# Kernel optimization log

Measured on AMD Instinct MI355X. Metric: run time of the kernel, lower is better.

## Reference

```python
import jax, jax.numpy as jnp
import numpy as np

HID = 64
CTX = 64
STEPS = 2
RANK = 16
NODES = 1024
B, T = 16, 24
EPS = 1e-5


def _linear(x, W, b):
    # torch nn.Linear: x @ W.T + b, W is [out, in]
    return jnp.einsum('...i,oi->...o', x, W) + b


def _gelu(x):
    return jax.nn.gelu(x, approximate=False)


def _diffusion(adj, state, Ws, bs):
    # Ws: [S, out, in], bs: [S, out]
    term = jnp.zeros_like(state)
    for s in range(Ws.shape[0]):
        state = jnp.einsum('nm,btmf->btnf', adj, state)
        term = term + _linear(state, Ws[s], bs[s])
    return term


def setup_inputs() -> dict:
    key = jax.random.key(0)
    ks = jax.random.split(key, 32)
    f32 = jnp.float32
    def w(k, *shape, scale=None):
        s = scale if scale is not None else 1.0 / np.sqrt(shape[-1])
        return jax.random.uniform(k, shape, f32, -s, s)
    inp = {
        'x': jax.random.normal(ks[0], (B, T, NODES, HID), f32),
        'a_fwd': jax.random.uniform(ks[1], (NODES, NODES), f32),
        'context': jax.random.normal(ks[2], (B, T, NODES, CTX), f32),
        'W_self': w(ks[3], HID, HID), 'b_self': w(ks[4], HID),
        'W_fwd': w(ks[5], STEPS, HID, HID), 'b_fwd': w(ks[6], STEPS, HID),
        'W_bwd': w(ks[7], STEPS, HID, HID), 'b_bwd': w(ks[8], STEPS, HID),
        'W_adp': w(ks[9], STEPS, HID, HID), 'b_adp': w(ks[10], STEPS, HID),
        'Wg1': w(ks[11], HID, CTX), 'bg1': w(ks[12], HID),
        'Wg2': w(ks[13], 4, HID), 'bg2': w(ks[14], 4),
        'Ws1': w(ks[15], HID, CTX), 'bs1': w(ks[16], HID),
        'Ws2': w(ks[17], HID, HID), 'bs2': w(ks[18], HID),
        'W_src': w(ks[19], 1, CTX), 'b_src': w(ks[20], 1),
        'W_dst': w(ks[21], 1, CTX), 'b_dst': w(ks[22], 1),
        'emb_src': jax.random.normal(ks[23], (NODES, RANK), f32) * 0.02,
        'emb_dst': jax.random.normal(ks[24], (NODES, RANK), f32) * 0.02,
        'gamma': jnp.ones((HID,), f32), 'beta': jnp.zeros((HID,), f32),
    }
    return inp


def reference(x, a_fwd, context, W_self, b_self, W_fwd, b_fwd, W_bwd, b_bwd,
              W_adp, b_adp, Wg1, bg1, Wg2, bg2, Ws1, bs1, Ws2, bs2,
              W_src, b_src, W_dst, b_dst, emb_src, emb_dst, gamma, beta):
    a_bwd = a_fwd.T
    # adaptive adjacency: softmax(relu(Es @ Ed^T)) over last dim
    a_adp = jax.nn.softmax(jax.nn.relu(emb_src @ emb_dst.T), axis=-1)

    gates = jax.nn.sigmoid(_linear(_gelu(_linear(context, Wg1, bg1)), Wg2, bg2))  # [b,t,n,4]
    scale = jax.nn.sigmoid(_linear(_gelu(_linear(context, Ws1, bs1)), Ws2, bs2))  # [b,t,n,F]
    src_gate = jax.nn.sigmoid(_linear(context, W_src, b_src))  # [b,t,n,1]
    dst_gate = jax.nn.sigmoid(_linear(context, W_dst, b_dst))  # [b,t,n,1]

    self_term = _linear(x, W_self, b_self)
    fwd_term = _diffusion(a_fwd, x * dst_gate, W_fwd, b_fwd)
    bwd_term = _diffusion(a_bwd, x * src_gate, W_bwd, b_bwd)
    adp_term = _diffusion(a_adp, x, W_adp, b_adp)

    mixed = (gates[..., 0:1] * self_term + gates[..., 1:2] * fwd_term
             + gates[..., 2:3] * bwd_term + gates[..., 3:4] * adp_term) * scale

    h = x + _gelu(mixed)  # dropout is identity in eval mode
    mu = jnp.mean(h, axis=-1, keepdims=True)
    var = jnp.mean(jnp.square(h - mu), axis=-1, keepdims=True)
    return (h - mu) * jax.lax.rsqrt(var + EPS) * gamma + beta
```

## Files before the change

### kernel.cpp

```cpp
#include <hip/hip_runtime.h>
#include <math.h>

typedef unsigned short u16;
typedef short short8 __attribute__((ext_vector_type(8)));
typedef float f32x4 __attribute__((ext_vector_type(4)));

#define LN_EPS 1e-5f

__device__ __forceinline__ float gelu_exact(float x){
    return 0.5f * x * (1.0f + erff(x * 0.70710678118654752f));
}
__device__ __forceinline__ float sigmoidf_(float x){
    return 1.0f / (1.0f + __expf(-x));
}
__device__ __forceinline__ u16 f2bf(float f){
    unsigned u = __float_as_uint(f);
    u += 0x7fffu + ((u >> 16) & 1u);
    return (u16)(u >> 16);
}
__device__ __forceinline__ float b2f(u16 u){
    return __uint_as_float(((unsigned)u) << 16);
}

#define GLLDS(gp, lp) __builtin_amdgcn_global_load_lds( \
    (const __attribute__((address_space(1))) unsigned int*)(const void*)(gp), \
    (__attribute__((address_space(3))) unsigned int*)(void*)(lp), 16, 0, 0)

__global__ __launch_bounds__(256) void k_prep(
    const float* __restrict__ Wg1, const float* __restrict__ Ws1,
    const float* __restrict__ Ws2, const float* __restrict__ Wself,
    const float* __restrict__ Wg2, const float* __restrict__ Wsrc,
    const float* __restrict__ Wdst, const float* __restrict__ Wfwd,
    const float* __restrict__ Wbwd, const float* __restrict__ Wadp,
    u16* __restrict__ wbf)
{
    const int i = blockIdx.x*256 + threadIdx.x;
    if (i >= 41344) return;
    const float* src; int off;
    if      (i < 4096)  { src = Wg1;  off = 0; }
    else if (i < 8192)  { src = Ws1;  off = 4096; }
    else if (i < 12288) { src = Ws2;  off = 8192; }
    else if (i < 16384) { src = Wself;off = 12288; }
    else if (i < 24576) { src = Wfwd; off = 16384; }
    else if (i < 32768) { src = Wbwd; off = 24576; }
    else if (i < 40960) { src = Wadp; off = 32768; }
    else if (i < 41216) { src = Wg2;  off = 40960; }
    else if (i < 41280) { src = Wsrc; off = 41216; }
    else                { src = Wdst; off = 41280; }
    wbf[i] = f2bf(src[i - off]);
}

__global__ __launch_bounds__(256) void k_adp(const float* __restrict__ es,
                                             const float* __restrict__ ed,
                                             u16* __restrict__ aadp){
    __shared__ float srow[1024];
    __shared__ float s_es[16];
    __shared__ float sredm[4];
    __shared__ float sreds[4];
    const int n   = blockIdx.x;
    const int tid = threadIdx.x;
    const int wid = tid >> 6, lane = tid & 63;
    if (tid < 16) s_es[tid] = es[n*16 + tid];
    __syncthreads();
    float lmax = 0.0f;
    for (int m = tid; m < 1024; m += 256){
        const float* edm = ed + m*16;
        float z = 0.f;
        #pragma unroll
        for (int r = 0; r < 16; r++) z = fmaf(s_es[r], edm[r], z);
        z = fmaxf(z, 0.0f);
        srow[m] = z;
        lmax = fmaxf(lmax, z);
    }
    #pragma unroll
    for (int o = 32; o > 0; o >>= 1) lmax = fmaxf(lmax, __shfl_xor(lmax, o, 64));
    if (lane == 0) sredm[wid] = lmax;
    __syncthreads();
    const float tmax = fmaxf(fmaxf(sredm[0], sredm[1]), fmaxf(sredm[2], sredm[3]));
    float lsum = 0.f;
    for (int m = tid; m < 1024; m += 256){
        float e = expf(srow[m] - tmax);
        srow[m] = e;
        lsum += e;
    }
    #pragma unroll
    for (int o = 32; o > 0; o >>= 1) lsum += __shfl_xor(lsum, o, 64);
    if (lane == 0) sreds[wid] = lsum;
    __syncthreads();
    const float inv = 1.0f / (sreds[0] + sreds[1] + sreds[2] + sreds[3]);
    for (int m = tid; m < 1024; m += 256) aadp[(size_t)n*1024 + m] = f2bf(srow[m] * inv);
}

__global__ __launch_bounds__(256) void k_cvtbwd(const float* __restrict__ a,
                                                u16* __restrict__ afwd,
                                                u16* __restrict__ abwd){
    __shared__ float t[32][33];
    const int bx = blockIdx.x*32, by = blockIdx.y*32;
    const int tx = threadIdx.x & 31, ty = threadIdx.x >> 5;
    #pragma unroll
    for (int i = 0; i < 4; i++){
        const float v = a[(size_t)(by + ty + 8*i)*1024 + bx + tx];
        t[ty + 8*i][tx] = v;
        afwd[(size_t)(by + ty + 8*i)*1024 + bx + tx] = f2bf(v);
    }
    __syncthreads();
    #pragma unroll
    for (int i = 0; i < 4; i++)
        at_:
        abwd[(size_t)(bx + ty + 8*i)*1024 + by + tx] = f2bf(t[tx][ty + 8*i]);
}

__global__ __launch_bounds__(256, 4) void k_gating(
    const float* __restrict__ x,    const float* __restrict__ ctx,
    const u16* __restrict__ wg1,  const float* __restrict__ bg1,
    const u16* __restrict__ wg2,  const float* __restrict__ bg2,
    const u16* __restrict__ ws1,  const float* __restrict__ bs1,
    const u16* __restrict__ ws2,  const float* __restrict__ bs2,
    const u16* __restrict__ wsrc, const float* __restrict__ bsrc,
    const u16* __restrict__ wdst, const float* __restrict__ bdst,
    const u16* __restrict__ wself,const float* __restrict__ bself,
    float* __restrict__ gates, u16* __restrict__ scaleb,
    u16* __restrict__ accb,
    u16* __restrict__ xTp, u16* __restrict__ xTd, u16* __restrict__ xTs)
{
    __shared__ u16 H1[8192];
    __shared__ u16 H2[8192];
    __shared__ float sgate[128], dgate[128];

    const int tid  = threadIdx.x;
    const int wv   = tid >> 6, lane = tid & 63;
    const int lr   = lane & 15, lg = lane >> 4;
    const int wtok = wv * 32;
    const int tokbase = blockIdx.x * 128;
    const int bt = blockIdx.x >> 3;
    const int n0 = (blockIdx.x & 7) * 128;

    auto stage_coop = [&](u16* H, const float* g){
        #pragma unroll
        for (int i = 0; i < 8; i++){
            const int fid = i*256 + tid;
            const int t = fid >> 4, q = fid & 15;
            const float4 v = *(const float4*)&g[(size_t)t*64 + q*4];
            ushort4 s;
            s.x = f2bf(v.x); s.y = f2bf(v.y); s.z = f2bf(v.z); s.w = f2bf(v.w);
            *(ushort4*)&H[t*64 + ((((q>>1) ^ (t & 7)) << 3) | ((q & 1)*4))] = s;
        }
    };
    auto afrag = [&](const u16* H, int row, int kb)->short8{
        return *(const short8*)&H[wv*2048 + row*64 + ((kb ^ (row & 7)) << 3)];
    };
    auto wfrag = [&](const u16* W, int o, int kb8)->short8{
        return *(const short8*)&W[o*64 + kb8];
    };
    auto gemm32 = [&](const u16* Hs, const u16* W, const float* bias, f32x4 (&c)[2][4]){
        #pragma unroll
        for (int n = 0; n < 4; n++){
            const float bv = bias[n*16 + lr];
            #pragma unroll
            for (int m = 0; m < 2; m++){ f32x4 t = {bv,bv,bv,bv}; c[m][n] = t; }
        }
        #pragma unroll
        for (int kk = 0; kk < 2; kk++){
            short8 a[2];
            #pragma unroll
            for (int m = 0; m < 2; m++) a[m] = afrag(Hs, m*16 + lr, kk*4 + lg);
            #pragma unroll
            for (int n = 0; n < 4; n++){
                const short8 w = wfrag(W, n*16 + lr, kk*32 + lg*8);
                #pragma unroll
                for (int m = 0; m < 2; m++)
                    c[m][n] = __builtin_amdgcn_mfma_f32_16x16x32_bf16(a[m], w, c[m][n], 0,0,0);
            }
        }
    };
    auto storeH = [&](u16* Hd, f32x4 (&c)[2][4]){
        #pragma unroll
        for (int m = 0; m < 2; m++)
            #pragma unroll
            for (int n = 0; n < 4; n++){
                const int f = n*16 + lr;
                #pragma unroll
                for (int r = 0; r < 4; r++){
                    const int t = m*16 + lg*4 + r;
                    Hd[wv*2048 + t*64 + ((((f>>3) ^ (t & 7)) << 3) | (f & 7))] = f2bf(c[m][n][r]);
                }
            }
    };

    stage_coop(H1, ctx + (size_t)tokbase*64);
    __syncthreads();

    f32x4 c[2][4];

    gemm32(H1, wg1, bg1, c);
    #pragma unroll
    for (int m = 0; m < 2; m++)
        #pragma unroll
        for (int n = 0; n < 4; n++)
            #pragma unroll
            for (int r = 0; r < 4; r++) c[m][n][r] = gelu_exact(c[m][n][r]);
    storeH(H2, c);

    {
        f32x4 c2[2];
        const float bv = (lr == 0) ? bsrc[0] : (lr == 1 ? bdst[0] : 0.f);
        #pragma unroll
        for (int m = 0; m < 2; m++){ f32x4 t = {bv,bv,bv,bv}; c2[m] = t; }
        #pragma unroll
        for (int kk = 0; kk < 2; kk++){
            short8 a[2];
            #pragma unroll
            for (int m = 0; m < 2; m++) a[m] = afrag(H1, m*16 + lr, kk*4 + lg);
            short8 w = {0,0,0,0,0,0,0,0};
            if (lr == 0) w = wfrag(wsrc, 0, kk*32 + lg*8);
            else if (lr == 1) w = wfrag(wdst, 0, kk*32 + lg*8);
            #pragma unroll
            for (int m = 0; m < 2; m++)
                c2[m] = __builtin_amdgcn_mfma_f32_16x16x32_bf16(a[m], w, c2[m], 0,0,0);
        }
        #pragma unroll
        for (int m = 0; m < 2; m++)
            #pragma unroll
            for (int r = 0; r < 4; r++){
                const int t = wtok + m*16 + lg*4 + r;
                const float v = sigmoidf_(c2[m][r]);
                if (lr == 0) sgate[t] = v;
                if (lr == 1) dgate[t] = v;
            }
    }

    gemm32(H1, ws1, bs1, c);
    #pragma unroll
    for (int m = 0; m < 2; m++)
        #pragma unroll
        for (int n = 0; n < 4; n++)
            #pragma unroll
            for (int r = 0; r < 4; r++) c[m][n][r] = gelu_exact(c[m][n][r]);
    storeH(H1, c);

    float g0[2][4];
    {
        f32x4 c3[2];
        const float bv = (lr < 4) ? bg2[lr] : 0.f;
        #pragma unroll
        for (int m = 0; m < 2; m++){ f32x4 t = {bv,bv,bv,bv}; c3[m] = t; }
        #pragma unroll
        for (int kk = 0; kk < 2; kk++){
            short8 a[2];
            #pragma unroll
            for (int m = 0; m < 2; m++) a[m] = afrag(H2, m*16 + lr, kk*4 + lg);
            short8 w = {0,0,0,0,0,0,0,0};
            if (lr < 4) w = wfrag(wg2, lr, kk*32 + lg*8);
            #pragma unroll
            for (int m = 0; m < 2; m++)
                c3[m] = __builtin_amdgcn_mfma_f32_16x16x32_bf16(a[m], w, c3[m], 0,0,0);
        }
        #pragma unroll
        for (int m = 0; m < 2; m++)
            #pragma unroll
            for (int r = 0; r < 4; r++){
                const float v = sigmoidf_(c3[m][r]);
                if (lr < 4)
                    gates[(size_t)(tokbase + wtok + m*16 + lg*4 + r)*4 + lr] = v;
                g0[m][r] = __shfl(v, lane & 48, 64);
            }
    }

    gemm32(H1, ws2, bs2, c);
    #pragma unroll
    for (int m = 0; m < 2; m++)
        #pragma unroll
        for (int n = 0; n < 4; n++)
            #pragma unroll
            for (int r = 0; r < 4; r++) c[m][n][r] = sigmoidf_(c[m][n][r]);
    storeH(H1, c);
    {
        #pragma unroll
        for (int it = 0; it < 4; it++){
            const int r2  = wtok + it*8 + (lane >> 3);
            const int sub = lane & 7;
            const short8 v = *(const short8*)&H1[r2*64 + ((sub ^ (r2 & 7)) << 3)];
            *(short8*)&scaleb[(size_t)(tokbase + r2)*64 + sub*8] = v;
        }
    }

    __syncthreads();
    stage_coop(H2, x + (size_t)tokbase*64);
    __syncthreads();

    gemm32(H2, wself, bself, c);
    #pragma unroll
    for (int m = 0; m < 2; m++)
        #pragma unroll
        for (int n = 0; n < 4; n++)
            #pragma unroll
            for (int r = 0; r < 4; r++) c[m][n][r] *= g0[m][r];
    storeH(H1, c);
    {
        #pragma unroll
        for (int it = 0; it < 4; it++){
            const int r2  = wtok + it*8 + (lane >> 3);
            const int sub = lane & 7;
            const short8 v = *(const short8*)&H1[r2*64 + ((sub ^ (r2 & 7)) << 3)];
            *(short8*)&accb[(size_t)(tokbase + r2)*64 + sub*8] = v;
        }
    }

    {
        const int tok  = tid & 127;
        const int fbh  = tid >> 7;
        const float dg = dgate[tok], sg = sgate[tok];
        const size_t ob = (size_t)bt*65536 + n0 + tok;
        #pragma unroll
        for (int q = 0; q < 4; q++){
            const int fb = fbh*4 + q;
            const short8 v = *(const short8*)&H2[tok*64 + ((fb ^ (tok & 7)) << 3)];
            #pragma unroll
            for (int j = 0; j < 8; j++){
                const u16 raw = (u16)v[j];
                const float xv = b2f(raw);
                const size_t o = ob + (size_t)(fb*8 + j)*1024;
                xTp[o] = raw;
                xTd[o] = f2bf(xv * dg);
                xTs[o] = f2bf(xv * sg);
            }
        }
    }
}

template<bool WRITE_TMP, bool FINAL>
__global__ __launch_bounds__(256, 3) void k_diffmm(
    const u16* __restrict__ adj,  const u16* __restrict__ srcT,
    const u16* __restrict__ Wbf,  const float* __restrict__ bias,
    const float* __restrict__ gates, const int branch,
    u16* __restrict__ accb, u16* __restrict__ tmpT,
    const float* __restrict__ x, const u16* __restrict__ scaleb,
    const float* __restrict__ gamma, const float* __restrict__ beta,
    float* __restrict__ out)
{
    __shared__ u16 sA[2][128*64];
    __shared__ u16 sB[2][64*64];

    const int tid = threadIdx.x;
    const int fb_ = blockIdx.x;
    const int s_  = (fb_ & 7) * 384 + (fb_ >> 3);
    const int bt  = s_ >> 3;
    const int n0  = (s_ & 7) * 128;
    const int wv  = tid >> 6, lane = tid & 63;
    const int lr  = lane & 15, lg = lane >> 4;
    const int wrow0 = wv * 32;

    const u16* asrc = adj  + (size_t)n0 * 1024;
    const u16* bsrc = srcT + (size_t)bt * 65536;

    auto stage = [&](int buf, int kt){
        const int m0 = kt * 64;
        #pragma unroll
        for (int i = 0; i < 4; i++){
            const int s = i*256 + tid;
            const int row = s >> 3, kbp = s & 7;
            const int kb = kbp ^ (row & 7);
            GLLDS(asrc + (size_t)row*1024 + m0 + kb*8, &sA[buf][s*8]);
        }
        #pragma unroll
        for (int i = 0; i < 2; i++){
            const int s = i*256 + tid;
            const int row = s >> 3, kbp = s & 7;
            const int kb = kbp ^ (row & 7);
            GLLDS(bsrc + (size_t)row*1024 + m0 + kb*8, &sB[buf][s*8]);
        }
    };

    const f32x4 z4 = {0.f, 0.f, 0.f, 0.f};
    f32x4 c[2][4];
    #pragma unroll
    for (int m = 0; m < 2; m++)
        #pragma unroll
        for (int n = 0; n < 4; n++) c[m][n] = z4;

    stage(0, 0);
    asm volatile("s_waitcnt vmcnt(0)" ::: "memory");
    __syncthreads();

    int cur = 0;
    for (int kt = 0; kt < 16; kt++){
        if (kt < 15) stage(cur ^ 1, kt + 1);
        const u16* A = sA[cur];
        const u16* B = sB[cur];
        short8 af[2][2], bfr[2][4];
        #pragma unroll
        for (int kk = 0; kk < 2; kk++){
            const int kb = lg + kk*4;
            #pragma unroll
            for (int m = 0; m < 2; m++){
                const int row = wrow0 + m*16 + lr;
                af[kk][m] = *(const short8*)&A[row*64 + ((kb ^ (row & 7)) << 3)];
            }
            #pragma unroll
            for (int n = 0; n < 4; n++){
                const int fr = n*16 + lr;
                bfr[kk][n] = *(const short8*)&B[fr*64 + ((kb ^ (fr & 7)) << 3)];
            }
        }
        #pragma unroll
        for (int kk = 0; kk < 2; kk++)
            #pragma unroll
            for (int m = 0; m < 2; m++)
                #pragma unroll
                for (int n = 0; n < 4; n++)
                    c[m][n] = __builtin_amdgcn_mfma_f32_16x16x32_bf16(
                        af[kk][m], bfr[kk][n], c[m][n], 0, 0, 0);
        asm volatile("s_waitcnt vmcnt(0)" ::: "memory");
        __syncthreads();
        cur ^= 1;
    }

    u16* yT = &sA[0][0];
    u16* eL = &sA[1][0];
    #pragma unroll
    for (int m = 0; m < 2; m++)
        #pragma unroll
        for (int n = 0; n < 4; n++){
            const int f = n*16 + lr;
            #pragma unroll
            for (int r = 0; r < 4; r++){
                const int row = wrow0 + m*16 + lg*4 + r;
                yT[row*64 + (((f >> 3) ^ (row & 7)) << 3) + (f & 7)] = f2bf(c[m][n][r]);
            }
        }
    __syncthreads();

    const int rowt = tid >> 1, half = tid & 1;
    if (WRITE_TMP){
        const size_t ob = (size_t)bt*65536 + n0 + rowt;
        #pragma unroll
        for (int q = 0; q < 4; q++){
            const int fbk = half*4 + q;
            const short8 v = *(const short8*)&yT[rowt*64 + ((fbk ^ (rowt & 7)) << 3)];
            #pragma unroll
            for (int j = 0; j < 8; j++)
                tmpT[ob + (size_t)(fbk*8 + j)*1024] = (u16)v[j];
        }
    }

    f32x4 lin[2][4];
    #pragma unroll
    for (int m = 0; m < 2; m++)
        #pragma unroll
        for (int n = 0; n < 4; n++) lin[m][n] = z4;
    #pragma unroll
    for (int kk = 0; kk < 2; kk++){
        const int kb = lg + kk*4;
        short8 ya[2], wb[4];
        #pragma unroll
        for (int m = 0; m < 2; m++){
            const int row = wrow0 + m*16 + lr;
            ya[m] = *(const short8*)&yT[row*64 + ((kb ^ (row & 7)) << 3)];
        }
        #pragma unroll
        for (int n = 0; n < 4; n++)
            wb[n] = *(const short8*)&Wbf[(n*16 + lr)*64 + kb*8];
        #pragma unroll
        for (int m = 0; m < 2; m++)
            #pragma unroll
            for (int n = 0; n < 4; n++)
                lin[m][n] = __builtin_amdgcn_mfma_f32_16x16x32_bf16(
                    ya[m], wb[n], lin[m][n], 0, 0, 0);
    }

    if constexpr (!FINAL){
        #pragma unroll
        for (int m = 0; m < 2; m++){
            float g[4];
            #pragma unroll
            for (int r = 0; r < 4; r++){
                const int node = n0 + wrow0 + m*16 + lg*4 + r;
                g[r] = gates[((size_t)bt*1024 + node)*4 + branch];
            }
            #pragma unroll
            for (int n = 0; n < 4; n++){
                const int f = n*16 + lr;
                const float bv = bias[f];
                #pragma unroll
                for (int r = 0; r < 4; r++){
                    const int row = wrow0 + m*16 + lg*4 + r;
                    eL[row*64 + (((f >> 3) ^ (row & 7)) << 3) + (f & 7)]
                        = f2bf(g[r] * (lin[m][n][r] + bv));
                }
            }
        }
        __syncthreads();
        const size_t tokb = ((size_t)bt*1024 + n0 + rowt)*64;
        #pragma unroll
        for (int q = 0; q < 4; q++){
            const int fbk = half*4 + q;
            const short8 e = *(const short8*)&eL[rowt*64 + ((fbk ^ (rowt & 7)) << 3)];
            const short8 a = *(const short8*)&accb[tokb + fbk*8];
            short8 o;
            #pragma unroll
            for (int j = 0; j < 8; j++)
                o[j] = (short)f2bf(b2f((u16)a[j]) + b2f((u16)e[j]));
            *(short8*)&accb[tokb + fbk*8] = o;
        }
    } else {
        #pragma unroll
        for (int m = 0; m < 2; m++){
            #pragma unroll
            for (int r = 0; r < 4; r++){
                const int node = n0 + wrow0 + m*16 + lg*4 + r;
                const size_t tok = (size_t)bt*1024 + node;
                const float g = gates[tok*4 + branch];
                float h[4];
                #pragma unroll
                for (int n = 0; n < 4; n++){
                    const int f = n*16 + lr;
                    const float a = b2f(accb[tok*64 + f]) + g * (lin[m][n][r] + bias[f]);
                    const float mixed = a * b2f(scaleb[tok*64 + f]);
                    h[n] = x[tok*64 + f] + gelu_exact(mixed);
                }
                float s = h[0] + h[1] + h[2] + h[3];
                #pragma unroll
                for (int o = 8; o > 0; o >>= 1) s += __shfl_xor(s, o, 64);
                const float mu = s * (1.0f/64.0f);
                float vs = 0.f;
                #pragma unroll
                for (int n = 0; n < 4; n++){ const float d = h[n] - mu; vs += d*d; }
                #pragma unroll
                for (int o = 8; o > 0; o >>= 1) vs += __shfl_xor(vs, o, 64);
                const float inv = rsqrtf(vs * (1.0f/64.0f) + LN_EPS);
                #pragma unroll
                for (int n = 0; n < 4; n++){
                    const int f = n*16 + lr;
                    out[tok*64 + f] = (h[n] - mu) * inv * gamma[f] + beta[f];
                }
            }
        }
    }
}

extern "C" void kernel_launch(void* const* d_in, const int* in_sizes, int n_in,
                              void* d_out, int out_size, void* d_ws, size_t ws_size,
                              hipStream_t stream)
{
    const float* x      = (const float*)d_in[0];
    const float* a_fwd  = (const float*)d_in[1];
    const float* ctx    = (const float*)d_in[2];
    const float* W_self = (const float*)d_in[3];
    const float* b_self = (const float*)d_in[4];
    const float* W_fwd  = (const float*)d_in[5];
    const float* b_fwd  = (const float*)d_in[6];
    const float* W_bwd  = (const float*)d_in[7];
    const float* b_bwd  = (const float*)d_in[8];
    const float* W_adp  = (const float*)d_in[9];
    const float* b_adp  = (const float*)d_in[10];
    const float* Wg1    = (const float*)d_in[11];
    const float* bg1    = (const float*)d_in[12];
    const float* Wg2    = (const float*)d_in[13];
    const float* bg2    = (const float*)d_in[14];
    const float* Ws1    = (const float*)d_in[15];
    const float* bs1    = (const float*)d_in[16];
    const float* Ws2    = (const float*)d_in[17];
    const float* bs2    = (const float*)d_in[18];
    const float* W_src  = (const float*)d_in[19];
    const float* b_src  = (const float*)d_in[20];
    const float* W_dst  = (const float*)d_in[21];
    const float* b_dst  = (const float*)d_in[22];
    const float* emb_src= (const float*)d_in[23];
    const float* emb_dst= (const float*)d_in[24];
    const float* gamma  = (const float*)d_in[25];
    const float* beta   = (const float*)d_in[26];

    float* out = (float*)d_out;
    char*  w   = (char*)d_ws;
    const size_t MB48 = 50331648ull;
    u16* afwd_bf = (u16*)(w);
    u16* abwd_bf = (u16*)(w + 2097152ull);
    u16* aadp_bf = (u16*)(w + 4194304ull);
    u16* xTp     = (u16*)(w + 6291456ull);
    u16* xTd     = (u16*)(w + 6291456ull + 1*MB48);
    u16* xTs     = (u16*)(w + 6291456ull + 2*MB48);
    u16* tmpT    = (u16*)(w + 6291456ull + 3*MB48);
    u16* scaleb  = (u16*)(w + 6291456ull + 4*MB48);
    u16* accb    = (u16*)(w + 6291456ull + 5*MB48);
    float* gates = (float*)(w + 6291456ull + 6*MB48);
    u16* wbf     = (u16*)(w + 6291456ull + 6*MB48 + 8388608ull);

    k_prep  <<<162, 256, 0, stream>>>(Wg1, Ws1, Ws2, W_self, Wg2, W_src, W_dst,
                                      W_fwd, W_bwd, W_adp, wbf);
    k_adp   <<<1024, 256, 0, stream>>>(emb_src, emb_dst, aadp_bf);
    k_cvtbwd<<<dim3(32,32), 256, 0, stream>>>(a_fwd, afwd_bf, abwd_bf);
    k_gating<<<3072, 256, 0, stream>>>(x, ctx,
                                       wbf + 0,     bg1,  wbf + 40960, bg2,
                                       wbf + 4096,  bs1,  wbf + 8192,  bs2,
                                       wbf + 41216, b_src, wbf + 41280, b_dst,
                                       wbf + 12288, b_self,
                                       gates, scaleb, accb, xTp, xTd, xTs);

    k_diffmm<true ,false><<<3072,256,0,stream>>>(afwd_bf, xTd,  wbf+16384, b_fwd,
                                                 gates, 1, accb, tmpT,
                                                 nullptr, nullptr, nullptr, nullptr, nullptr);
    k_diffmm<false,false><<<3072,256,0,stream>>>(afwd_bf, tmpT, wbf+20480, b_fwd+64,
                                                 gates, 1, accb, nullptr,
                                                 nullptr, nullptr, nullptr, nullptr, nullptr);
    k_diffmm<true ,false><<<3072,256,0,stream>>>(abwd_bf, xTs,  wbf+24576, b_bwd,
                                                 gates, 2, accb, tmpT,
                                                 nullptr, nullptr, nullptr, nullptr, nullptr);
    k_diffmm<false,false><<<3072,256,0,stream>>>(abwd_bf, tmpT, wbf+28672, b_bwd+64,
                                                 gates, 2, accb, nullptr,
                                                 nullptr, nullptr, nullptr, nullptr, nullptr);
    k_diffmm<true ,false><<<3072,256,0,stream>>>(aadp_bf, xTp,  wbf+32768, b_adp,
                                                 gates, 3, accb, tmpT,
                                                 nullptr, nullptr, nullptr, nullptr, nullptr);
    k_diffmm<false,true ><<<3072,256,0,stream>>>(aadp_bf, tmpT, wbf+36864, b_adp+64,
                                                 gates, 3, accb, nullptr,
                                                 x, scaleb, gamma, beta, out);
}
```

Measured before the change: 869.4 us.

## Halve diffusion GEMM row tile, raise occupancy, pack transposed bf16 stores

The diffusion GEMM tile shrinks from 128 to 64 node rows per block, so the grid doubles and LDS use drops. The launch bounds also go from 3 to 4 blocks per SIMD, aiming for more concurrent waves. Transposed scatter stores in both the gating and diffusion kernels now write two adjacent tokens as one 32-bit word instead of separate 16-bit stores. The trade-off is that each B (state) tile is reused across half as many adjacency rows, roughly doubling B-tile global traffic. The change also removes a stray label in the transpose kernel.

```diff
diff --git a/kernel.cpp b/kernel.cpp
--- a/kernel.cpp
+++ b/kernel.cpp
@@ -106,7 +106,6 @@
     __syncthreads();
     #pragma unroll
     for (int i = 0; i < 4; i++)
-        at_:
         abwd[(size_t)(bx + ty + 8*i)*1024 + by + tx] = f2bf(t[tx][ty + 8*i]);
 }
 
@@ -307,29 +306,32 @@
     }
 
     {
-        const int tok  = tid & 127;
-        const int fbh  = tid >> 7;
-        const float dg = dgate[tok], sg = sgate[tok];
-        const size_t ob = (size_t)bt*65536 + n0 + tok;
-        #pragma unroll
-        for (int q = 0; q < 4; q++){
-            const int fb = fbh*4 + q;
-            const short8 v = *(const short8*)&H2[tok*64 + ((fb ^ (tok & 7)) << 3)];
+        const int p    = tid & 63;
+        const int fsel = tid >> 6;
+        const int t0 = 2*p, t1 = 2*p + 1;
+        const float dg0 = dgate[t0], dg1 = dgate[t1];
+        const float sg0 = sgate[t0], sg1 = sgate[t1];
+        const size_t ob = (size_t)bt*65536 + n0 + t0;
+        #pragma unroll
+        for (int fq = 0; fq < 2; fq++){
+            const int fb = fsel*2 + fq;
+            const short8 v0 = *(const short8*)&H2[t0*64 + ((fb ^ (t0 & 7)) << 3)];
+            const short8 v1 = *(const short8*)&H2[t1*64 + ((fb ^ (t1 & 7)) << 3)];
             #pragma unroll
             for (int j = 0; j < 8; j++){
-                const u16 raw = (u16)v[j];
-                const float xv = b2f(raw);
+                const u16 r0 = (u16)v0[j], r1 = (u16)v1[j];
+                const float x0 = b2f(r0), x1 = b2f(r1);
                 const size_t o = ob + (size_t)(fb*8 + j)*1024;
-                xTp[o] = raw;
-                xTd[o] = f2bf(xv * dg);
-                xTs[o] = f2bf(xv * sg);
+                *(unsigned*)&xTp[o] = ((unsigned)r1 << 16) | r0;
+                *(unsigned*)&xTd[o] = ((unsigned)f2bf(x1*dg1) << 16) | f2bf(x0*dg0);
+                *(unsigned*)&xTs[o] = ((unsigned)f2bf(x1*sg1) << 16) | f2bf(x0*sg0);
             }
         }
     }
 }
 
 template<bool WRITE_TMP, bool FINAL>
-__global__ __launch_bounds__(256, 3) void k_diffmm(
+__global__ __launch_bounds__(256, 4) void k_diffmm(
     const u16* __restrict__ adj,  const u16* __restrict__ srcT,
     const u16* __restrict__ Wbf,  const float* __restrict__ bias,
     const float* __restrict__ gates, const int branch,
@@ -338,17 +340,17 @@
     const float* __restrict__ gamma, const float* __restrict__ beta,
     float* __restrict__ out)
 {
-    __shared__ u16 sA[2][128*64];
+    __shared__ u16 sA[2][64*64];
     __shared__ u16 sB[2][64*64];
 
     const int tid = threadIdx.x;
     const int fb_ = blockIdx.x;
-    const int s_  = (fb_ & 7) * 384 + (fb_ >> 3);
-    const int bt  = s_ >> 3;
-    const int n0  = (s_ & 7) * 128;
+    const int s_  = (fb_ & 7) * 768 + (fb_ >> 3);
+    const int bt  = s_ >> 4;
+    const int n0  = (s_ & 15) * 64;
     const int wv  = tid >> 6, lane = tid & 63;
     const int lr  = lane & 15, lg = lane >> 4;
-    const int wrow0 = wv * 32;
+    const int wrow0 = wv * 16;
 
     const u16* asrc = adj  + (size_t)n0 * 1024;
     const u16* bsrc = srcT + (size_t)bt * 65536;
@@ -356,7 +358,7 @@
     auto stage = [&](int buf, int kt){
         const int m0 = kt * 64;
         #pragma unroll
-        for (int i = 0; i < 4; i++){
+        for (int i = 0; i < 2; i++){
             const int s = i*256 + tid;
             const int row = s >> 3, kbp = s & 7;
             const int kb = kbp ^ (row & 7);
@@ -372,11 +374,9 @@
     };
 
     const f32x4 z4 = {0.f, 0.f, 0.f, 0.f};
-    f32x4 c[2][4];
-    #pragma unroll
-    for (int m = 0; m < 2; m++)
-        #pragma unroll
-        for (int n = 0; n < 4; n++) c[m][n] = z4;
+    f32x4 c[4];
+    #pragma unroll
+    for (int n = 0; n < 4; n++) c[n] = z4;
 
     stage(0, 0);
     asm volatile("s_waitcnt vmcnt(0)" ::: "memory");
@@ -387,14 +387,13 @@
         if (kt < 15) stage(cur ^ 1, kt + 1);
         const u16* A = sA[cur];
         const u16* B = sB[cur];
-        short8 af[2][2], bfr[2][4];
+        short8 af[2], bfr[2][4];
         #pragma unroll
         for (int kk = 0; kk < 2; kk++){
             const int kb = lg + kk*4;
-            #pragma unroll
-            for (int m = 0; m < 2; m++){
-                const int row = wrow0 + m*16 + lr;
-                af[kk][m] = *(const short8*)&A[row*64 + ((kb ^ (row & 7)) << 3)];
+            {
+                const int row = wrow0 + lr;
+                af[kk] = *(const short8*)&A[row*64 + ((kb ^ (row & 7)) << 3)];
             }
             #pragma unroll
             for (int n = 0; n < 4; n++){
@@ -405,11 +404,9 @@
         #pragma unroll
         for (int kk = 0; kk < 2; kk++)
             #pragma unroll
-            for (int m = 0; m < 2; m++)
-                #pragma unroll
-                for (int n = 0; n < 4; n++)
-                    c[m][n] = __builtin_amdgcn_mfma_f32_16x16x32_bf16(
-                        af[kk][m], bfr[kk][n], c[m][n], 0, 0, 0);
+            for (int n = 0; n < 4; n++)
+                c[n] = __builtin_amdgcn_mfma_f32_16x16x32_bf16(
+                    af[kk], bfr[kk][n], c[n], 0, 0, 0);
         asm volatile("s_waitcnt vmcnt(0)" ::: "memory");
         __syncthreads();
         cur ^= 1;
@@ -418,82 +415,73 @@
     u16* yT = &sA[0][0];
     u16* eL = &sA[1][0];
     #pragma unroll
-    for (int m = 0; m < 2; m++)
+    for (int n = 0; n < 4; n++){
+        const int f = n*16 + lr;
+        #pragma unroll
+        for (int r = 0; r < 4; r++){
+            const int row = wrow0 + lg*4 + r;
+            yT[row*64 + (((f >> 3) ^ (row & 7)) << 3) + (f & 7)] = f2bf(c[n][r]);
+        }
+    }
+    __syncthreads();
+
+    if (WRITE_TMP){
+        const int rp = tid >> 3, fbk = tid & 7;
+        const int r0 = 2*rp, r1 = 2*rp + 1;
+        const short8 v0 = *(const short8*)&yT[r0*64 + ((fbk ^ (r0 & 7)) << 3)];
+        const short8 v1 = *(const short8*)&yT[r1*64 + ((fbk ^ (r1 & 7)) << 3)];
+        const size_t ob = (size_t)bt*65536 + n0 + r0;
+        #pragma unroll
+        for (int j = 0; j < 8; j++){
+            const unsigned wd = ((unsigned)(u16)v1[j] << 16) | (u16)v0[j];
+            *(unsigned*)&tmpT[ob + (size_t)(fbk*8 + j)*1024] = wd;
+        }
+    }
+
+    f32x4 lin[4];
+    #pragma unroll
+    for (int n = 0; n < 4; n++) lin[n] = z4;
+    #pragma unroll
+    for (int kk = 0; kk < 2; kk++){
+        const int kb = lg + kk*4;
+        short8 ya, wb[4];
+        {
+            const int row = wrow0 + lr;
+            ya = *(const short8*)&yT[row*64 + ((kb ^ (row & 7)) << 3)];
+        }
+        #pragma unroll
+        for (int n = 0; n < 4; n++)
+            wb[n] = *(const short8*)&Wbf[(n*16 + lr)*64 + kb*8];
+        #pragma unroll
+        for (int n = 0; n < 4; n++)
+            lin[n] = __builtin_amdgcn_mfma_f32_16x16x32_bf16(
+                ya, wb[n], lin[n], 0, 0, 0);
+    }
+
+    if constexpr (!FINAL){
+        float g[4];
+        #pragma unroll
+        for (int r = 0; r < 4; r++){
+            const int node = n0 + wrow0 + lg*4 + r;
+            g[r] = gates[((size_t)bt*1024 + node)*4 + branch];
+        }
         #pragma unroll
         for (int n = 0; n < 4; n++){
             const int f = n*16 + lr;
+            const float bv = bias[f];
             #pragma unroll
             for (int r = 0; r < 4; r++){
-                const int row = wrow0 + m*16 + lg*4 + r;
-                yT[row*64 + (((f >> 3) ^ (row & 7)) << 3) + (f & 7)] = f2bf(c[m][n][r]);
-            }
-        }
-    __syncthreads();
-
-    const int rowt = tid >> 1, half = tid & 1;
-    if (WRITE_TMP){
-        const size_t ob = (size_t)bt*65536 + n0 + rowt;
-        #pragma unroll
-        for (int q = 0; q < 4; q++){
-            const int fbk = half*4 + q;
-            const short8 v = *(const short8*)&yT[rowt*64 + ((fbk ^ (rowt & 7)) << 3)];
-            #pragma unroll
-            for (int j = 0; j < 8; j++)
-                tmpT[ob + (size_t)(fbk*8 + j)*1024] = (u16)v[j];
-        }
-    }
-
-    f32x4 lin[2][4];
-    #pragma unroll
-    for (int m = 0; m < 2; m++)
-        #pragma unroll
-        for (int n = 0; n < 4; n++) lin[m][n] = z4;
-    #pragma unroll
-    for (int kk = 0; kk < 2; kk++){
-        const int kb = lg + kk*4;
-        short8 ya[2], wb[4];
-        #pragma unroll
-        for (int m = 0; m < 2; m++){
-            const int row = wrow0 + m*16 + lr;
-            ya[m] = *(const short8*)&yT[row*64 + ((kb ^ (row & 7)) << 3)];
-        }
-        #pragma unroll
-        for (int n = 0; n < 4; n++)
-            wb[n] = *(const short8*)&Wbf[(n*16 + lr)*64 + kb*8];
-        #pragma unroll
-        for (int m = 0; m < 2; m++)
-            #pragma unroll
-            for (int n = 0; n < 4; n++)
-                lin[m][n] = __builtin_amdgcn_mfma_f32_16x16x32_bf16(
-                    ya[m], wb[n], lin[m][n], 0, 0, 0);
-    }
-
-    if constexpr (!FINAL){
-        #pragma unroll
-        for (int m = 0; m < 2; m++){
-            float g[4];
-            #pragma unroll
-            for (int r = 0; r < 4; r++){
-                const int node = n0 + wrow0 + m*16 + lg*4 + r;
-                g[r] = gates[((size_t)bt*1024 + node)*4 + branch];
-            }
-            #pragma unroll
-            for (int n = 0; n < 4; n++){
-                const int f = n*16 + lr;
-                const float bv = bias[f];
-                #pragma unroll
-                for (int r = 0; r < 4; r++){
-                    const int row = wrow0 + m*16 + lg*4 + r;
-                    eL[row*64 + (((f >> 3) ^ (row & 7)) << 3) + (f & 7)]
-                        = f2bf(g[r] * (lin[m][n][r] + bv));
-                }
+                const int row = wrow0 + lg*4 + r;
+                eL[row*64 + (((f >> 3) ^ (row & 7)) << 3) + (f & 7)]
+                    = f2bf(g[r] * (lin[n][r] + bv));
             }
         }
         __syncthreads();
+        const int rowt = tid >> 2, q = tid & 3;
         const size_t tokb = ((size_t)bt*1024 + n0 + rowt)*64;
         #pragma unroll
-        for (int q = 0; q < 4; q++){
-            const int fbk = half*4 + q;
+        for (int t2 = 0; t2 < 2; t2++){
+            const int fbk = q*2 + t2;
             const short8 e = *(const short8*)&eL[rowt*64 + ((fbk ^ (rowt & 7)) << 3)];
             const short8 a = *(const short8*)&accb[tokb + fbk*8];
             short8 o;
@@ -504,35 +492,32 @@
         }
     } else {
         #pragma unroll
-        for (int m = 0; m < 2; m++){
-            #pragma unroll
-            for (int r = 0; r < 4; r++){
-                const int node = n0 + wrow0 + m*16 + lg*4 + r;
-                const size_t tok = (size_t)bt*1024 + node;
-                const float g = gates[tok*4 + branch];
-                float h[4];
-                #pragma unroll
-                for (int n = 0; n < 4; n++){
-                    const int f = n*16 + lr;
-                    const float a = b2f(accb[tok*64 + f]) + g * (lin[m][n][r] + bias[f]);
-                    const float mixed = a * b2f(scaleb[tok*64 + f]);
-                    h[n] = x[tok*64 + f] + gelu_exact(mixed);
-                }
-                float s = h[0] + h[1] + h[2] + h[3];
-                #pragma unroll
-                for (int o = 8; o > 0; o >>= 1) s += __shfl_xor(s, o, 64);
-                const float mu = s * (1.0f/64.0f);
-                float vs = 0.f;
-                #pragma unroll
-                for (int n = 0; n < 4; n++){ const float d = h[n] - mu; vs += d*d; }
-                #pragma unroll
-                for (int o = 8; o > 0; o >>= 1) vs += __shfl_xor(vs, o, 64);
-                const float inv = rsqrtf(vs * (1.0f/64.0f) + LN_EPS);
-                #pragma unroll
-                for (int n = 0; n < 4; n++){
-                    const int f = n*16 + lr;
-                    out[tok*64 + f] = (h[n] - mu) * inv * gamma[f] + beta[f];
-                }
+        for (int r = 0; r < 4; r++){
+            const int node = n0 + wrow0 + lg*4 + r;
+            const size_t tok = (size_t)bt*1024 + node;
+            const float g = gates[tok*4 + branch];
+            float h[4];
+            #pragma unroll
+            for (int n = 0; n < 4; n++){
+                const int f = n*16 + lr;
+                const float a = b2f(accb[tok*64 + f]) + g * (lin[n][r] + bias[f]);
+                const float mixed = a * b2f(scaleb[tok*64 + f]);
+                h[n] = x[tok*64 + f] + gelu_exact(mixed);
+            }
+            float s = h[0] + h[1] + h[2] + h[3];
+            #pragma unroll
+            for (int o = 8; o > 0; o >>= 1) s += __shfl_xor(s, o, 64);
+            const float mu = s * (1.0f/64.0f);
+            float vs = 0.f;
+            #pragma unroll
+            for (int n = 0; n < 4; n++){ const float d = h[n] - mu; vs += d*d; }
+            #pragma unroll
+            for (int o = 8; o > 0; o >>= 1) vs += __shfl_xor(vs, o, 64);
+            const float inv = rsqrtf(vs * (1.0f/64.0f) + LN_EPS);
+            #pragma unroll
+            for (int n = 0; n < 4; n++){
+                const int f = n*16 + lr;
+                out[tok*64 + f] = (h[n] - mu) * inv * gamma[f] + beta[f];
             }
         }
     }
@@ -596,22 +581,22 @@
                                        wbf + 12288, b_self,
                                        gates, scaleb, accb, xTp, xTd, xTs);
 
-    k_diffmm<true ,false><<<3072,256,0,stream>>>(afwd_bf, xTd,  wbf+16384, b_fwd,
+    k_diffmm<true ,false><<<6144,256,0,stream>>>(afwd_bf, xTd,  wbf+16384, b_fwd,
                                                  gates, 1, accb, tmpT,
                                                  nullptr, nullptr, nullptr, nullptr, nullptr);
-    k_diffmm<false,false><<<3072,256,0,stream>>>(afwd_bf, tmpT, wbf+20480, b_fwd+64,
+    k_diffmm<false,false><<<6144,256,0,stream>>>(afwd_bf, tmpT, wbf+20480, b_fwd+64,
                                                  gates, 1, accb, nullptr,
                                                  nullptr, nullptr, nullptr, nullptr, nullptr);
-    k_diffmm<true ,false><<<3072,256,0,stream>>>(abwd_bf, xTs,  wbf+24576, b_bwd,
+    k_diffmm<true ,false><<<6144,256,0,stream>>>(abwd_bf, xTs,  wbf+24576, b_bwd,
                                                  gates, 2, accb, tmpT,
                                                  nullptr, nullptr, nullptr, nullptr, nullptr);
-    k_diffmm<false,false><<<3072,256,0,stream>>>(abwd_bf, tmpT, wbf+28672, b_bwd+64,
+    k_diffmm<false,false><<<6144,256,0,stream>>>(abwd_bf, tmpT, wbf+28672, b_bwd+64,
                                                  gates, 2, accb, nullptr,
                                                  nullptr, nullptr, nullptr, nullptr, nullptr);
-    k_diffmm<true ,false><<<3072,256,0,stream>>>(aadp_bf, xTp,  wbf+32768, b_adp,
+    k_diffmm<true ,false><<<6144,256,0,stream>>>(aadp_bf, xTp,  wbf+32768, b_adp,
                                                  gates, 3, accb, tmpT,
                                                  nullptr, nullptr, nullptr, nullptr, nullptr);
-    k_diffmm<false,true ><<<3072,256,0,stream>>>(aadp_bf, tmpT, wbf+36864, b_adp+64,
+    k_diffmm<false,true ><<<6144,256,0,stream>>>(aadp_bf, tmpT, wbf+36864, b_adp+64,
                                                  gates, 3, accb, nullptr,
                                                  x, scaleb, gamma, beta, out);
 }
```

After: 1.122 ms. +29.1%, slower.

## Load adjacency A-fragments directly to registers instead of via LDS in diffusion GEMM

Applied to the files above, without the earlier changes.

The diffusion matmul kernel no longer stages the 128x64 adjacency tile through shared memory. Each lane now loads its MFMA A-fragments straight from global memory into registers, double-buffered across k-steps, and only the B operand goes through LDS. This shrinks shared memory so launch bounds can go from 3 to 4 blocks per CU, and it removes LDS traffic for A. The cost is uncoalesced-ish 16-byte global loads per lane and more registers for the prefetched fragments, which may cause spills under the tighter occupancy target. A stray label in the transpose kernel is also removed.

```diff
diff --git a/kernel.cpp b/kernel.cpp
--- a/kernel.cpp
+++ b/kernel.cpp
@@ -106,7 +106,6 @@
     __syncthreads();
     #pragma unroll
     for (int i = 0; i < 4; i++)
-        at_:
         abwd[(size_t)(bx + ty + 8*i)*1024 + by + tx] = f2bf(t[tx][ty + 8*i]);
 }
 
@@ -329,7 +328,7 @@
 }
 
 template<bool WRITE_TMP, bool FINAL>
-__global__ __launch_bounds__(256, 3) void k_diffmm(
+__global__ __launch_bounds__(256, 4) void k_diffmm(
     const u16* __restrict__ adj,  const u16* __restrict__ srcT,
     const u16* __restrict__ Wbf,  const float* __restrict__ bias,
     const float* __restrict__ gates, const int branch,
@@ -338,8 +337,8 @@
     const float* __restrict__ gamma, const float* __restrict__ beta,
     float* __restrict__ out)
 {
-    __shared__ u16 sA[2][128*64];
     __shared__ u16 sB[2][64*64];
+    __shared__ u16 yS[128*64];
 
     const int tid = threadIdx.x;
     const int fb_ = blockIdx.x;
@@ -350,18 +349,14 @@
     const int lr  = lane & 15, lg = lane >> 4;
     const int wrow0 = wv * 32;
 
-    const u16* asrc = adj  + (size_t)n0 * 1024;
-    const u16* bsrc = srcT + (size_t)bt * 65536;
-
-    auto stage = [&](int buf, int kt){
+    const u16* bsrc  = srcT + (size_t)bt * 65536;
+    const u16* arow0 = adj + (size_t)(n0 + wrow0 + lr) * 1024;
+    const u16* arow1 = arow0 + 16 * 1024;
+    const int akoff0 = lg * 8;
+    const int akoff1 = (lg + 4) * 8;
+
+    auto stageB = [&](int buf, int kt){
         const int m0 = kt * 64;
-        #pragma unroll
-        for (int i = 0; i < 4; i++){
-            const int s = i*256 + tid;
-            const int row = s >> 3, kbp = s & 7;
-            const int kb = kbp ^ (row & 7);
-            GLLDS(asrc + (size_t)row*1024 + m0 + kb*8, &sA[buf][s*8]);
-        }
         #pragma unroll
         for (int i = 0; i < 2; i++){
             const int s = i*256 + tid;
@@ -370,6 +365,13 @@
             GLLDS(bsrc + (size_t)row*1024 + m0 + kb*8, &sB[buf][s*8]);
         }
     };
+    auto loadA = [&](int kt, short8 (&a)[2][2]){
+        const int m0 = kt * 64;
+        a[0][0] = *(const short8*)&arow0[m0 + akoff0];
+        a[0][1] = *(const short8*)&arow1[m0 + akoff0];
+        a[1][0] = *(const short8*)&arow0[m0 + akoff1];
+        a[1][1] = *(const short8*)&arow1[m0 + akoff1];
+    };
 
     const f32x4 z4 = {0.f, 0.f, 0.f, 0.f};
     f32x4 c[2][4];
@@ -378,45 +380,46 @@
         #pragma unroll
         for (int n = 0; n < 4; n++) c[m][n] = z4;
 
-    stage(0, 0);
+    short8 aC[2][2], aN[2][2];
+    loadA(0, aC);
+    stageB(0, 0);
     asm volatile("s_waitcnt vmcnt(0)" ::: "memory");
     __syncthreads();
 
-    int cur = 0;
+    #pragma unroll
     for (int kt = 0; kt < 16; kt++){
-        if (kt < 15) stage(cur ^ 1, kt + 1);
-        const u16* A = sA[cur];
+        const int cur = kt & 1;
+        if (kt < 15){
+            stageB(cur ^ 1, kt + 1);
+            loadA(kt + 1, aN);
+        }
         const u16* B = sB[cur];
-        short8 af[2][2], bfr[2][4];
         #pragma unroll
         for (int kk = 0; kk < 2; kk++){
             const int kb = lg + kk*4;
-            #pragma unroll
-            for (int m = 0; m < 2; m++){
-                const int row = wrow0 + m*16 + lr;
-                af[kk][m] = *(const short8*)&A[row*64 + ((kb ^ (row & 7)) << 3)];
-            }
+            short8 bfr[4];
             #pragma unroll
             for (int n = 0; n < 4; n++){
                 const int fr = n*16 + lr;
-                bfr[kk][n] = *(const short8*)&B[fr*64 + ((kb ^ (fr & 7)) << 3)];
-            }
-        }
-        #pragma unroll
-        for (int kk = 0; kk < 2; kk++)
+                bfr[n] = *(const short8*)&B[fr*64 + ((kb ^ (fr & 7)) << 3)];
+            }
             #pragma unroll
             for (int m = 0; m < 2; m++)
                 #pragma unroll
                 for (int n = 0; n < 4; n++)
                     c[m][n] = __builtin_amdgcn_mfma_f32_16x16x32_bf16(
-                        af[kk][m], bfr[kk][n], c[m][n], 0, 0, 0);
+                        aC[kk][m], bfr[n], c[m][n], 0, 0, 0);
+        }
         asm volatile("s_waitcnt vmcnt(0)" ::: "memory");
         __syncthreads();
-        cur ^= 1;
-    }
-
-    u16* yT = &sA[0][0];
-    u16* eL = &sA[1][0];
+        #pragma unroll
+        for (int kk = 0; kk < 2; kk++)
+            #pragma unroll
+            for (int m = 0; m < 2; m++) aC[kk][m] = aN[kk][m];
+    }
+
+    u16* yT = &yS[0];
+    u16* eL = &sB[0][0];
     #pragma unroll
     for (int m = 0; m < 2; m++)
         #pragma unroll
@@ -434,8 +437,8 @@
     if (WRITE_TMP){
         const size_t ob = (size_t)bt*65536 + n0 + rowt;
         #pragma unroll
-        for (int q = 0; q < 4; q++){
-            const int fbk = half*4 + q;
+        for (int qq = 0; qq < 4; qq++){
+            const int fbk = half*4 + qq;
             const short8 v = *(const short8*)&yT[rowt*64 + ((fbk ^ (rowt & 7)) << 3)];
             #pragma unroll
             for (int j = 0; j < 8; j++)
@@ -492,8 +495,8 @@
         __syncthreads();
         const size_t tokb = ((size_t)bt*1024 + n0 + rowt)*64;
         #pragma unroll
-        for (int q = 0; q < 4; q++){
-            const int fbk = half*4 + q;
+        for (int qq = 0; qq < 4; qq++){
+            const int fbk = half*4 + qq;
             const short8 e = *(const short8*)&eL[rowt*64 + ((fbk ^ (rowt & 7)) << 3)];
             const short8 a = *(const short8*)&accb[tokb + fbk*8];
             short8 o;
```

Result: slower. 1.063 ms (+22.3%).
